# Kernel tuning notes

Measured on AMD Instinct MI355X. Metric: run time of the kernel, lower is better.

Reference implementation:

```python
import jax, jax.numpy as jnp
import numpy as np

VOCAB = 200000
E = 128   # embedding_size
H = 128   # lstm_hidden_size
OH = 1024 # output_hidden_size
B = 256   # pair batch
L = 256   # per-sentence length


def setup_inputs() -> dict:
    key = jax.random.key(0)
    ks = jax.random.split(key, 8)
    return {
        "s1": jax.random.randint(ks[0], (B, L), 0, VOCAB, dtype=jnp.int32),
        "s2": jax.random.randint(ks[1], (B, L), 0, VOCAB, dtype=jnp.int32),
        "emb_W": jax.random.normal(ks[2], (VOCAB, E), jnp.float32) * 0.1,
        "W_fwd": jax.random.normal(ks[3], (E + H, 4 * H), jnp.float32) * 0.1,
        "b_fwd": jnp.zeros((4 * H,), jnp.float32),
        "W_bwd": jax.random.normal(ks[4], (E + H, 4 * H), jnp.float32) * 0.1,
        "b_bwd": jnp.zeros((4 * H,), jnp.float32),
        "W_mid": jax.random.normal(ks[5], (4 * H, OH), jnp.float32) * 0.1,
        "b_mid": jnp.zeros((OH,), jnp.float32),
        "W_out": jax.random.normal(ks[6], (OH, 1), jnp.float32) * 0.1,
        "b_out": jnp.zeros((1,), jnp.float32),
    }


def _reverse_sequence(x, lens):
    # x: [N, T, ...]; reverse first lens[n] steps of each row (tf.reverse_sequence)
    T = x.shape[1]
    t = jnp.arange(T)[None, :]                      # [1, T]
    idx = jnp.where(t < lens[:, None], lens[:, None] - 1 - t, t)  # [N, T]
    return jnp.take_along_axis(x, idx[..., None], axis=1)


def _lstm(x, lens, W, b):
    # x: [N, T, E]; BasicLSTMCell with forget_bias=1.0, zeros past lens (dynamic_rnn)
    N, T, _ = x.shape
    x_tm = jnp.swapaxes(x, 0, 1)                    # [T, N, E]
    ts = jnp.arange(T)
    h0 = jnp.zeros((N, H), x.dtype)
    c0 = jnp.zeros((N, H), x.dtype)

    def step(carry, inp):
        h, c = carry
        xt, t = inp
        z = jnp.concatenate([xt, h], axis=-1) @ W + b
        i, j, f, o = jnp.split(z, 4, axis=-1)
        nc = c * jax.nn.sigmoid(f + 1.0) + jax.nn.sigmoid(i) * jnp.tanh(j)
        nh = jnp.tanh(nc) * jax.nn.sigmoid(o)
        m = (t < lens)[:, None]
        return (jnp.where(m, nh, h), jnp.where(m, nc, c)), jnp.where(m, nh, 0.0)

    _, ys = jax.lax.scan(step, (h0, c0), (x_tm, ts))
    return jnp.swapaxes(ys, 0, 1)                   # [N, T, H]


def reference(s1, s2, emb_W, W_fwd, b_fwd, W_bwd, b_bwd, W_mid, b_mid, W_out, b_out):
    # input_concat: [B, 2L] -> [2B, L]
    inp = jnp.concatenate([s1, s2], axis=1).reshape(-1, L)       # [2B, L]
    lens = jnp.sum(inp != 0, axis=1)                              # count_nonzero
    emb = emb_W[inp]                                              # [2B, L, E]

    out_f = _lstm(emb, lens, W_fwd, b_fwd)                        # [2B, L, H]
    # backward dir: reverse_sequence -> lstm -> reverse_sequence (bidirectional_dynamic_rnn)
    out_b = _reverse_sequence(_lstm(_reverse_sequence(emb, lens), lens, W_bwd, b_bwd), lens)
    # original graph applies an extra full tf.reverse on the backward output
    lstm_out = jnp.concatenate([out_f, jnp.flip(out_b, axis=1)], axis=2)  # [2B, L, 2H]

    seq_vec = jnp.mean(lstm_out, axis=1)                          # [2B, 2H]
    feats = seq_vec.reshape(-1, 4 * H)                            # [B, 4H]
    hid = jax.nn.relu(feats @ W_mid + b_mid)
    logits = hid @ W_out + b_out                                  # [B, 1]
    return jax.nn.sigmoid(logits).reshape(-1)                     # [B]
```

## Files before the change

kernel.cpp:

```cpp
#include <hip/hip_runtime.h>
#include <stdint.h>
#include <stddef.h>


typedef short short8 __attribute__((ext_vector_type(8)));
typedef float f32x4  __attribute__((ext_vector_type(4)));

#define LSEQ    256
#define NCOL    512
#define RSTRIDE 544
#define CBUF    (4 * RSTRIDE)

__device__ __forceinline__ unsigned short f2bf(float f) {
    unsigned u = __builtin_bit_cast(unsigned, f);
    u += 0x7fffu + ((u >> 16) & 1u);
    return (unsigned short)(u >> 16);
}
__device__ __forceinline__ float sigm(float x) {
    float t = __builtin_amdgcn_exp2f(-1.4426950408889634f * x);
    return __builtin_amdgcn_rcpf(1.0f + t);
}

__global__ __launch_bounds__(1024)
void bilstm_kernel(const int* __restrict__ s1, const int* __restrict__ s2,
                   const float* __restrict__ embW,
                   const float* __restrict__ Wf, const float* __restrict__ bf_,
                   const float* __restrict__ Wb, const float* __restrict__ bb_,
                   float* __restrict__ seqvec ) {
    const int tid  = threadIdx.x;
    const int lane = tid & 63;
    const int wave = tid >> 6;
    const int dir   = blockIdx.x & 1;
    const int sbase = (blockIdx.x >> 1) * 4;

    const float* __restrict__ W    = dir ? Wb  : Wf;
    const float* __restrict__ bias = dir ? bb_ : bf_;

    __shared__ char In[2 * CBUF];
    __shared__ int  tokL[4][LSEQ];
    __shared__ int  lenS[4];

    if (tid * 16 < 2 * CBUF) *(short8*)(In + tid * 16) = (short8)0;

    int mylen = 0;
    if (wave < 4) {
        const int n = sbase + wave;
        const int* src = (n & 1) ? (s2 + (size_t)(n >> 1) * LSEQ)
                                 : (s1 + (size_t)(n >> 1) * LSEQ);
        const int4 tk = *(const int4*)(src + lane * 4);
        *(int4*)&tokL[wave][lane * 4] = tk;
        int cnt = (tk.x != 0) + (tk.y != 0) + (tk.z != 0) + (tk.w != 0);
        #pragma unroll
        for (int s = 1; s < 64; s <<= 1) cnt += __shfl_xor(cnt, s, 64);
        mylen = cnt;
        if (lane == 0) lenS[wave] = cnt;
    }
    __syncthreads();

    const int c = lane & 15;
    const int g = lane >> 4;
    const int unit = wave * 8 + (c & 7);
    const int colnt0 = (c < 8) ? unit : (128 + unit);
    const int colnt1 = (c < 8) ? (256 + unit) : (384 + unit);
    const int kb = g * 8;

    short8 wfrag[8][2];
    #pragma unroll
    for (int kk = 0; kk < 8; ++kk) {
        #pragma unroll
        for (int nt = 0; nt < 2; ++nt) {
            const int col = nt ? colnt1 : colnt0;
            short8 v;
            #pragma unroll
            for (int j = 0; j < 8; ++j)
                v[j] = (short)f2bf(W[(size_t)(kk * 32 + kb + j) * NCOL + col]);
            f32x4 tmp = __builtin_bit_cast(f32x4, v);
            asm volatile("" : "+v"(tmp));
            wfrag[kk][nt] = __builtin_bit_cast(short8, tmp);
        }
    }
    const float bias0 = bias[colnt0];
    const float bias1 = bias[colnt1] + ((c < 8) ? 1.0f : 0.0f);

    const bool  lo  = (c < 8);
    const float km0 = lo ? -1.4426950408889634f : -2.8853900817779268f;
    const float am0 = lo ? 1.0f : 2.0f;
    const float bm0 = lo ? 0.0f : -1.0f;
    const float KM1 = -1.4426950408889634f;
    const float KM2 = -2.8853900817779268f;

    const int abase = (c & 3) * RSTRIDE + g * 16;
    const int hoff  = g * RSTRIDE + 256 + unit * 2;
    const int xoff  = wave * RSTRIDE + lane * 4;

    if (wave < 4) {
        const int idx0 = dir ? ((0 < mylen) ? (mylen - 1) : 0) : 0;
        const int tk = tokL[wave][idx0];
        const float2 xv = *(const float2*)(embW + (size_t)tk * 128 + lane * 2);
        *(unsigned*)(In + xoff) =
            (unsigned)f2bf(xv.x) | ((unsigned)f2bf(xv.y) << 16);
    }
    __syncthreads();

    const int lenv = lenS[g];
    float cs = 0.f, sm = 0.f, hs = 0.f;

    auto STEP = [&](int t, const char* bR, char* bW) {
        float2 xv;
        if (wave < 4) {
            const int tp  = (t + 1 < LSEQ) ? t + 1 : LSEQ - 1;
            const int idx = dir ? ((tp < mylen) ? (mylen - 1 - tp) : tp) : tp;
            const int tk  = tokL[wave][idx];
            xv = *(const float2*)(embW + (size_t)tk * 128 + lane * 2);
        }

        f32x4 a0 = {bias0, bias0, bias0, bias0};
        f32x4 a1 = {bias1, bias1, bias1, bias1};
        f32x4 b0 = {0.f, 0.f, 0.f, 0.f};
        f32x4 b1 = {0.f, 0.f, 0.f, 0.f};
        #pragma unroll
        for (int kk = 0; kk < 8; kk += 2) {
            const short8 af0 = *(const short8*)(bR + abase + kk * 64);
            const short8 af1 = *(const short8*)(bR + abase + kk * 64 + 64);
            a0 = __builtin_amdgcn_mfma_f32_16x16x32_bf16(af0, wfrag[kk][0],     a0, 0, 0, 0);
            a1 = __builtin_amdgcn_mfma_f32_16x16x32_bf16(af0, wfrag[kk][1],     a1, 0, 0, 0);
            b0 = __builtin_amdgcn_mfma_f32_16x16x32_bf16(af1, wfrag[kk + 1][0], b0, 0, 0, 0);
            b1 = __builtin_amdgcn_mfma_f32_16x16x32_bf16(af1, wfrag[kk + 1][1], b1, 0, 0, 0);
        }
        const f32x4 z0 = a0 + b0;
        const f32x4 z1 = a1 + b1;

        const float zc0 = (g < 2) ? ((g == 0) ? z0[0] : z0[1])
                                  : ((g == 2) ? z0[2] : z0[3]);
        const float zc1 = (g < 2) ? ((g == 0) ? z1[0] : z1[1])
                                  : ((g == 2) ? z1[2] : z1[3]);

        const float e0  = __builtin_amdgcn_exp2f(km0 * zc0);
        const float g0v = am0 * __builtin_amdgcn_rcpf(1.0f + e0) + bm0;
        const float e1  = __builtin_amdgcn_exp2f(KM1 * zc1);
        const float g1v = __builtin_amdgcn_rcpf(1.0f + e1);

        const float jt = __shfl_xor(g0v, 8, 64);
        const float ot = __shfl_xor(g1v, 8, 64);

        const bool  v  = (t < lenv);
        const float nc = cs * g1v + g0v * jt;
        const float er = __builtin_amdgcn_exp2f(KM2 * nc);
        const float th = 2.0f * __builtin_amdgcn_rcpf(1.0f + er) - 1.0f;
        const float nh = th * ot;
        cs = v ? nc : cs;
        sm += v ? nh : 0.0f;
        hs = v ? nh : hs;

        if (c < 8) *(unsigned short*)(bW + hoff) = f2bf(hs);
        if (wave < 4)
            *(unsigned*)(bW + xoff) =
                (unsigned)f2bf(xv.x) | ((unsigned)f2bf(xv.y) << 16);
        __syncthreads();
    };

    for (int t = 0; t < LSEQ; t += 2) {
        STEP(t,     In,        In + CBUF);
        STEP(t + 1, In + CBUF, In);
    }

    if (c < 8)
        seqvec[(size_t)(sbase + g) * 256 + dir * 128 + unit] = sm * (1.0f / 256.0f);
}

__global__ __launch_bounds__(1024)
void mlp_kernel(const float* __restrict__ feats,
                const float* __restrict__ Wm, const float* __restrict__ bm,
                const float* __restrict__ Wo, const float* __restrict__ bo,
                float* __restrict__ out) {
    const int tid = threadIdx.x;
    const int p   = blockIdx.x;
    __shared__ float fe[512];
    __shared__ float red[16];

    if (tid < 512) fe[tid] = feats[(size_t)p * 512 + tid];
    __syncthreads();

    float a0 = 0.f, a1 = 0.f, a2 = 0.f, a3 = 0.f;
    #pragma unroll 4
    for (int k = 0; k < 512; k += 4) {
        a0 = fmaf(Wm[(size_t)(k + 0) * 1024 + tid], fe[k + 0], a0);
        a1 = fmaf(Wm[(size_t)(k + 1) * 1024 + tid], fe[k + 1], a1);
        a2 = fmaf(Wm[(size_t)(k + 2) * 1024 + tid], fe[k + 2], a2);
        a3 = fmaf(Wm[(size_t)(k + 3) * 1024 + tid], fe[k + 3], a3);
    }
    const float h = fmaxf((a0 + a1) + (a2 + a3) + bm[tid], 0.f);
    float part = h * Wo[tid];

    #pragma unroll
    for (int s = 1; s < 64; s <<= 1) part += __shfl_xor(part, s, 64);
    if ((tid & 63) == 0) red[tid >> 6] = part;
    __syncthreads();
    if (tid < 64) {
        float v = (tid < 16) ? red[tid] : 0.f;
        #pragma unroll
        for (int s = 1; s < 16; s <<= 1) v += __shfl_xor(v, s, 64);
        if (tid == 0) out[p] = sigm(v + bo[0]);
    }
}

extern "C" void kernel_launch(void* const* d_in, const int* in_sizes, int n_in,
                              void* d_out, int out_size, void* d_ws, size_t ws_size,
                              hipStream_t stream) {
    const int*   s1   = (const int*)d_in[0];
    const int*   s2   = (const int*)d_in[1];
    const float* embW = (const float*)d_in[2];
    const float* Wf   = (const float*)d_in[3];
    const float* bf_  = (const float*)d_in[4];
    const float* Wb   = (const float*)d_in[5];
    const float* bb_  = (const float*)d_in[6];
    const float* Wm   = (const float*)d_in[7];
    const float* bm   = (const float*)d_in[8];
    const float* Wo   = (const float*)d_in[9];
    const float* bo   = (const float*)d_in[10];

    float* seqvec = (float*)d_ws;

    bilstm_kernel<<<256, 1024, 0, stream>>>(s1, s2, embW, Wf, bf_, Wb, bb_, seqvec);
    mlp_kernel<<<256, 1024, 0, stream>>>(seqvec, Wm, bm, Wo, bo, (float*)d_out);
}
```

Before: 398.2 us.

## Split LSTM x/h projections to precompute next-step input gates off critical path

Separates the input projection (x·Wx) from the recurrent projection (h·Wh), with x and h in separate double buffers. The next step's x contribution is computed with MFMAs while the current step's gate nonlinearities run, so only four dependent MFMAs stay on the serial recurrence path. The change also pre-reverses token indices into shared memory, permutes the gate columns so one shuffle carries i*j, and restructures the MLP into a column-tiled partial kernel plus a small finalize kernel. The cost is extra register pressure, which the added launch-bounds hint tries to contain, and one more kernel launch.

Result: faster. 383.7 us (-3.7%).

```diff
diff --git a/kernel.cpp b/kernel.cpp
--- a/kernel.cpp
+++ b/kernel.cpp
@@ -6,10 +6,12 @@
 typedef short short8 __attribute__((ext_vector_type(8)));
 typedef float f32x4  __attribute__((ext_vector_type(4)));
 
-#define LSEQ    256
-#define NCOL    512
-#define RSTRIDE 544
-#define CBUF    (4 * RSTRIDE)
+#define LSEQ 256
+#define NCOL 512
+#define RS   288
+#define ABUF (4 * RS)
+
+#define MFMA(A, B, C) __builtin_amdgcn_mfma_f32_16x16x32_bf16((A), (B), (C), 0, 0, 0)
 
 __device__ __forceinline__ unsigned short f2bf(float f) {
     unsigned u = __builtin_bit_cast(unsigned, f);
@@ -21,7 +23,7 @@
     return __builtin_amdgcn_rcpf(1.0f + t);
 }
 
-__global__ __launch_bounds__(1024)
+__global__ __launch_bounds__(1024, 4)
 void bilstm_kernel(const int* __restrict__ s1, const int* __restrict__ s2,
                    const float* __restrict__ embW,
                    const float* __restrict__ Wf, const float* __restrict__ bf_,
@@ -36,11 +38,17 @@
     const float* __restrict__ W    = dir ? Wb  : Wf;
     const float* __restrict__ bias = dir ? bb_ : bf_;
 
-    __shared__ char In[2 * CBUF];
-    __shared__ int  tokL[4][LSEQ];
+    __shared__ char xb[2 * ABUF];
+    __shared__ char hb[2 * ABUF];
+    __shared__ int  tokRaw[4][LSEQ];
+    __shared__ int  tokR[4][LSEQ];
     __shared__ int  lenS[4];
 
-    if (tid * 16 < 2 * CBUF) *(short8*)(In + tid * 16) = (short8)0;
+    const int c = lane & 15;
+    const int g = lane >> 4;
+    const int unit = wave * 8 + (c & 7);
+
+    if (tid < ABUF / 16) *(short8*)(hb + ABUF + tid * 16) = (short8)0;
 
     int mylen = 0;
     if (wave < 4) {
@@ -48,21 +56,29 @@
         const int* src = (n & 1) ? (s2 + (size_t)(n >> 1) * LSEQ)
                                  : (s1 + (size_t)(n >> 1) * LSEQ);
         const int4 tk = *(const int4*)(src + lane * 4);
-        *(int4*)&tokL[wave][lane * 4] = tk;
+        *(int4*)&tokRaw[wave][lane * 4] = tk;
         int cnt = (tk.x != 0) + (tk.y != 0) + (tk.z != 0) + (tk.w != 0);
         #pragma unroll
         for (int s = 1; s < 64; s <<= 1) cnt += __shfl_xor(cnt, s, 64);
         mylen = cnt;
         if (lane == 0) lenS[wave] = cnt;
-    }
-    __syncthreads();
-
-    const int c = lane & 15;
-    const int g = lane >> 4;
-    const int unit = wave * 8 + (c & 7);
-    const int colnt0 = (c < 8) ? unit : (128 + unit);
-    const int colnt1 = (c < 8) ? (256 + unit) : (384 + unit);
-    const int kb = g * 8;
+        #pragma unroll
+        for (int r = 0; r < 4; ++r) {
+            const int t   = r * 64 + lane;
+            const int idx = dir ? ((t < mylen) ? (mylen - 1 - t) : t) : t;
+            tokR[wave][t] = tokRaw[wave][idx];
+        }
+        #pragma unroll
+        for (int s = 0; s < 2; ++s) {
+            const int tk2 = tokR[wave][s];
+            const float2 xv = *(const float2*)(embW + (size_t)tk2 * 128 + lane * 2);
+            *(unsigned*)(xb + s * ABUF + wave * RS + lane * 4) =
+                (unsigned)f2bf(xv.x) | ((unsigned)f2bf(xv.y) << 16);
+        }
+    }
+
+    const int colnt0 = (c < 8) ? unit : (256 + unit);
+    const int colnt1 = (c < 8) ? (128 + unit) : (384 + unit);
 
     short8 wfrag[8][2];
     #pragma unroll
@@ -73,135 +89,161 @@
             short8 v;
             #pragma unroll
             for (int j = 0; j < 8; ++j)
-                v[j] = (short)f2bf(W[(size_t)(kk * 32 + kb + j) * NCOL + col]);
+                v[j] = (short)f2bf(W[(size_t)(kk * 32 + g * 8 + j) * NCOL + col]);
             f32x4 tmp = __builtin_bit_cast(f32x4, v);
             asm volatile("" : "+v"(tmp));
             wfrag[kk][nt] = __builtin_bit_cast(short8, tmp);
         }
     }
-    const float bias0 = bias[colnt0];
-    const float bias1 = bias[colnt1] + ((c < 8) ? 1.0f : 0.0f);
-
-    const bool  lo  = (c < 8);
-    const float km0 = lo ? -1.4426950408889634f : -2.8853900817779268f;
-    const float am0 = lo ? 1.0f : 2.0f;
-    const float bm0 = lo ? 0.0f : -1.0f;
-    const float KM1 = -1.4426950408889634f;
+    const float b0s = bias[colnt0] + ((c >= 8) ? 1.0f : 0.0f);
+    const float b1s = bias[colnt1];
+    const f32x4 biasv0 = {b0s, b0s, b0s, b0s};
+    const f32x4 biasv1 = {b1s, b1s, b1s, b1s};
+
+    const float km1 = (c < 8) ? -2.8853900817779268f : -1.4426950408889634f;
+    const float a1c = (c < 8) ? 2.0f : 1.0f;
+    const float b1c = (c < 8) ? -1.0f : 0.0f;
+    const float KM0 = -1.4426950408889634f;
     const float KM2 = -2.8853900817779268f;
 
-    const int abase = (c & 3) * RSTRIDE + g * 16;
-    const int hoff  = g * RSTRIDE + 256 + unit * 2;
-    const int xoff  = wave * RSTRIDE + lane * 4;
-
-    if (wave < 4) {
-        const int idx0 = dir ? ((0 < mylen) ? (mylen - 1) : 0) : 0;
-        const int tk = tokL[wave][idx0];
-        const float2 xv = *(const float2*)(embW + (size_t)tk * 128 + lane * 2);
-        *(unsigned*)(In + xoff) =
-            (unsigned)f2bf(xv.x) | ((unsigned)f2bf(xv.y) << 16);
+    const int ard = (c & 3) * RS + g * 16;
+    const int hwr = g * RS + unit * 2;
+    const int xst = wave * RS + lane * 4;
+
+    __syncthreads();
+
+    f32x4 zxa, zxb;
+    {
+        const short8 x0 = *(const short8*)(xb + ard);
+        const short8 x1 = *(const short8*)(xb + ard + 64);
+        const short8 x2 = *(const short8*)(xb + ard + 128);
+        const short8 x3 = *(const short8*)(xb + ard + 192);
+        zxa = MFMA(x0, wfrag[0][0], biasv0);  zxb = MFMA(x0, wfrag[0][1], biasv1);
+        zxa = MFMA(x1, wfrag[1][0], zxa);     zxb = MFMA(x1, wfrag[1][1], zxb);
+        zxa = MFMA(x2, wfrag[2][0], zxa);     zxb = MFMA(x2, wfrag[2][1], zxb);
+        zxa = MFMA(x3, wfrag[3][0], zxa);     zxb = MFMA(x3, wfrag[3][1], zxb);
     }
     __syncthreads();
 
     const int lenv = lenS[g];
     float cs = 0.f, sm = 0.f, hs = 0.f;
 
-    auto STEP = [&](int t, const char* bR, char* bW) {
+    auto STEP = [&](int t, const char* hR, char* hW, const char* xR, char* xW) {
         float2 xv;
         if (wave < 4) {
-            const int tp  = (t + 1 < LSEQ) ? t + 1 : LSEQ - 1;
-            const int idx = dir ? ((tp < mylen) ? (mylen - 1 - tp) : tp) : tp;
-            const int tk  = tokL[wave][idx];
+            const int tp = (t + 2 < LSEQ) ? t + 2 : LSEQ - 1;
+            const int tk = tokR[wave][tp];
             xv = *(const float2*)(embW + (size_t)tk * 128 + lane * 2);
         }
 
-        f32x4 a0 = {bias0, bias0, bias0, bias0};
-        f32x4 a1 = {bias1, bias1, bias1, bias1};
-        f32x4 b0 = {0.f, 0.f, 0.f, 0.f};
-        f32x4 b1 = {0.f, 0.f, 0.f, 0.f};
-        #pragma unroll
-        for (int kk = 0; kk < 8; kk += 2) {
-            const short8 af0 = *(const short8*)(bR + abase + kk * 64);
-            const short8 af1 = *(const short8*)(bR + abase + kk * 64 + 64);
-            a0 = __builtin_amdgcn_mfma_f32_16x16x32_bf16(af0, wfrag[kk][0],     a0, 0, 0, 0);
-            a1 = __builtin_amdgcn_mfma_f32_16x16x32_bf16(af0, wfrag[kk][1],     a1, 0, 0, 0);
-            b0 = __builtin_amdgcn_mfma_f32_16x16x32_bf16(af1, wfrag[kk + 1][0], b0, 0, 0, 0);
-            b1 = __builtin_amdgcn_mfma_f32_16x16x32_bf16(af1, wfrag[kk + 1][1], b1, 0, 0, 0);
-        }
-        const f32x4 z0 = a0 + b0;
-        const f32x4 z1 = a1 + b1;
-
-        const float zc0 = (g < 2) ? ((g == 0) ? z0[0] : z0[1])
-                                  : ((g == 2) ? z0[2] : z0[3]);
-        const float zc1 = (g < 2) ? ((g == 0) ? z1[0] : z1[1])
-                                  : ((g == 2) ? z1[2] : z1[3]);
-
-        const float e0  = __builtin_amdgcn_exp2f(km0 * zc0);
-        const float g0v = am0 * __builtin_amdgcn_rcpf(1.0f + e0) + bm0;
-        const float e1  = __builtin_amdgcn_exp2f(KM1 * zc1);
-        const float g1v = __builtin_amdgcn_rcpf(1.0f + e1);
-
-        const float jt = __shfl_xor(g0v, 8, 64);
-        const float ot = __shfl_xor(g1v, 8, 64);
+        const short8 h0 = *(const short8*)(hR + ard);
+        const short8 h1 = *(const short8*)(hR + ard + 64);
+        const short8 h2 = *(const short8*)(hR + ard + 128);
+        const short8 h3 = *(const short8*)(hR + ard + 192);
+        f32x4 a = MFMA(h0, wfrag[4][0], zxa);
+        f32x4 b = MFMA(h0, wfrag[4][1], zxb);
+        a = MFMA(h1, wfrag[5][0], a);  b = MFMA(h1, wfrag[5][1], b);
+        a = MFMA(h2, wfrag[6][0], a);  b = MFMA(h2, wfrag[6][1], b);
+        a = MFMA(h3, wfrag[7][0], a);  b = MFMA(h3, wfrag[7][1], b);
+
+        const float zc0 = (g < 2) ? ((g == 0) ? a[0] : a[1])
+                                  : ((g == 2) ? a[2] : a[3]);
+        const float zc1 = (g < 2) ? ((g == 0) ? b[0] : b[1])
+                                  : ((g == 2) ? b[2] : b[3]);
+
+        const short8 x0 = *(const short8*)(xR + ard);
+        const short8 x1 = *(const short8*)(xR + ard + 64);
+        const short8 x2 = *(const short8*)(xR + ard + 128);
+        const short8 x3 = *(const short8*)(xR + ard + 192);
+
+        const float e0  = __builtin_amdgcn_exp2f(KM0 * zc0);
+        const float g0v = __builtin_amdgcn_rcpf(1.0f + e0);
+        const float e1  = __builtin_amdgcn_exp2f(km1 * zc1);
+        const float g1v = a1c * __builtin_amdgcn_rcpf(1.0f + e1) + b1c;
+        const float pr  = g0v * g1v;
+        const float prx = __shfl_xor(pr, 8, 64);
+
+        zxa = MFMA(x0, wfrag[0][0], biasv0);  zxb = MFMA(x0, wfrag[0][1], biasv1);
+        zxa = MFMA(x1, wfrag[1][0], zxa);     zxb = MFMA(x1, wfrag[1][1], zxb);
+        zxa = MFMA(x2, wfrag[2][0], zxa);     zxb = MFMA(x2, wfrag[2][1], zxb);
+        zxa = MFMA(x3, wfrag[3][0], zxa);     zxb = MFMA(x3, wfrag[3][1], zxb);
 
         const bool  v  = (t < lenv);
-        const float nc = cs * g1v + g0v * jt;
+        const float nc = cs * g0v + prx;
         const float er = __builtin_amdgcn_exp2f(KM2 * nc);
         const float th = 2.0f * __builtin_amdgcn_rcpf(1.0f + er) - 1.0f;
-        const float nh = th * ot;
+        const float nh = th * g1v;
         cs = v ? nc : cs;
         sm += v ? nh : 0.0f;
         hs = v ? nh : hs;
 
-        if (c < 8) *(unsigned short*)(bW + hoff) = f2bf(hs);
+        if (c >= 8) *(unsigned short*)(hW + hwr) = f2bf(hs);
         if (wave < 4)
-            *(unsigned*)(bW + xoff) =
+            *(unsigned*)(xW + xst) =
                 (unsigned)f2bf(xv.x) | ((unsigned)f2bf(xv.y) << 16);
         __syncthreads();
     };
 
-    for (int t = 0; t < LSEQ; t += 2) {
-        STEP(t,     In,        In + CBUF);
-        STEP(t + 1, In + CBUF, In);
-    }
-
-    if (c < 8)
+    for (int tt = 0; tt < LSEQ; tt += 2) {
+        STEP(tt,     hb + ABUF, hb,        xb + ABUF, xb);
+        STEP(tt + 1, hb,        hb + ABUF, xb,        xb + ABUF);
+    }
+
+    if (c >= 8)
         seqvec[(size_t)(sbase + g) * 256 + dir * 128 + unit] = sm * (1.0f / 256.0f);
 }
 
-__global__ __launch_bounds__(1024)
-void mlp_kernel(const float* __restrict__ feats,
-                const float* __restrict__ Wm, const float* __restrict__ bm,
-                const float* __restrict__ Wo, const float* __restrict__ bo,
-                float* __restrict__ out) {
-    const int tid = threadIdx.x;
-    const int p   = blockIdx.x;
-    __shared__ float fe[512];
-    __shared__ float red[16];
-
-    if (tid < 512) fe[tid] = feats[(size_t)p * 512 + tid];
+__global__ __launch_bounds__(256)
+void mlp_part(const float* __restrict__ feats,
+              const float* __restrict__ Wm, const float* __restrict__ bm,
+              const float* __restrict__ Wo,
+              float* __restrict__ partials ) {
+    const int tid  = threadIdx.x;
+    const int lane = tid & 63;
+    const int ct   = blockIdx.x & 3;
+    const int p0   = (blockIdx.x >> 2) * 4;
+    const int pair = p0 + (tid >> 6);
+    const int col4 = ct * 256 + lane * 4;
+    __shared__ float fe[4][512];
+
+    {
+        float* fef = &fe[0][0];
+        const float* src = feats + (size_t)p0 * 512;
+        *(float4*)&fef[tid * 8]     = *(const float4*)(src + tid * 8);
+        *(float4*)&fef[tid * 8 + 4] = *(const float4*)(src + tid * 8 + 4);
+    }
     __syncthreads();
 
-    float a0 = 0.f, a1 = 0.f, a2 = 0.f, a3 = 0.f;
-    #pragma unroll 4
+    f32x4 ac0 = {0,0,0,0}, ac1 = {0,0,0,0}, ac2 = {0,0,0,0}, ac3 = {0,0,0,0};
     for (int k = 0; k < 512; k += 4) {
-        a0 = fmaf(Wm[(size_t)(k + 0) * 1024 + tid], fe[k + 0], a0);
-        a1 = fmaf(Wm[(size_t)(k + 1) * 1024 + tid], fe[k + 1], a1);
-        a2 = fmaf(Wm[(size_t)(k + 2) * 1024 + tid], fe[k + 2], a2);
-        a3 = fmaf(Wm[(size_t)(k + 3) * 1024 + tid], fe[k + 3], a3);
-    }
-    const float h = fmaxf((a0 + a1) + (a2 + a3) + bm[tid], 0.f);
-    float part = h * Wo[tid];
+        const f32x4 w0 = *(const f32x4*)(Wm + (size_t)(k + 0) * 1024 + col4);
+        const f32x4 w1 = *(const f32x4*)(Wm + (size_t)(k + 1) * 1024 + col4);
+        const f32x4 w2 = *(const f32x4*)(Wm + (size_t)(k + 2) * 1024 + col4);
+        const f32x4 w3 = *(const f32x4*)(Wm + (size_t)(k + 3) * 1024 + col4);
+        ac0 += w0 * fe[pair - p0][k + 0];
+        ac1 += w1 * fe[pair - p0][k + 1];
+        ac2 += w2 * fe[pair - p0][k + 2];
+        ac3 += w3 * fe[pair - p0][k + 3];
+    }
+    const f32x4 acc = (ac0 + ac1) + (ac2 + ac3);
+    const f32x4 bm4 = *(const f32x4*)(bm + col4);
+    const f32x4 wo4 = *(const f32x4*)(Wo + col4);
+    float part = 0.f;
+    #pragma unroll
+    for (int q = 0; q < 4; ++q)
+        part += fmaxf(acc[q] + bm4[q], 0.f) * wo4[q];
 
     #pragma unroll
     for (int s = 1; s < 64; s <<= 1) part += __shfl_xor(part, s, 64);
-    if ((tid & 63) == 0) red[tid >> 6] = part;
-    __syncthreads();
-    if (tid < 64) {
-        float v = (tid < 16) ? red[tid] : 0.f;
-        #pragma unroll
-        for (int s = 1; s < 16; s <<= 1) v += __shfl_xor(v, s, 64);
-        if (tid == 0) out[p] = sigm(v + bo[0]);
-    }
+    if (lane == 0) partials[ct * 256 + pair] = part;
+}
+
+__global__ __launch_bounds__(256)
+void mlp_fin(const float* __restrict__ partials,
+             const float* __restrict__ bo, float* __restrict__ out) {
+    const int p = threadIdx.x;
+    out[p] = sigm(partials[p] + partials[256 + p] + partials[512 + p] +
+                  partials[768 + p] + bo[0]);
 }
 
 extern "C" void kernel_launch(void* const* d_in, const int* in_sizes, int n_in,
@@ -219,8 +261,10 @@
     const float* Wo   = (const float*)d_in[9];
     const float* bo   = (const float*)d_in[10];
 
-    float* seqvec = (float*)d_ws;
+    float* seqvec   = (float*)d_ws;
+    float* partials = seqvec + 512 * 256;
 
     bilstm_kernel<<<256, 1024, 0, stream>>>(s1, s2, embW, Wf, bf_, Wb, bb_, seqvec);
-    mlp_kernel<<<256, 1024, 0, stream>>>(seqvec, Wm, bm, Wo, bo, (float*)d_out);
-}
+    mlp_part<<<256, 256, 0, stream>>>(seqvec, Wm, bm, Wo, partials);
+    mlp_fin<<<1, 256, 0, stream>>>(partials, bo, (float*)d_out);
+}
```
